# Optimization experiments

Measured on AMD Instinct MI355X. Metric: run time of the kernel, lower is better.

The kernel has to match this reference:

```python
import jax, jax.numpy as jnp
import numpy as np

D = 1024       # d_model
DR = 1024      # d_rec
FFN = 4096     # ffn_inner
K = 4          # conv_kernel
B, T = 2, 4096
CHUNK = 64
EPS = 1e-6


def setup_inputs() -> dict:
    key = jax.random.key(0)
    ks = jax.random.split(key, 8)
    s = lambda k, shape, scale: jax.random.normal(k, shape, jnp.float32) * scale
    db = np.zeros((DR,), np.float32)
    q = DR // 4
    db[:q] = -2.2
    db[q:3 * q] = 0.0
    db[3 * q:] = 4.6
    return {
        "x": s(ks[0], (B, T, D), 1.0),
        "pre_norm_w": jnp.ones((D,), jnp.float32),
        "conv_w": s(ks[1], (D, 1, K), 0.3),
        "conv_b": jnp.zeros((D,), jnp.float32),
        "w_a": s(ks[2], (DR, D), 0.02),
        "w_i": s(ks[3], (DR, D), 0.02),
        "w_v": s(ks[4], (DR, D), 0.02),
        "out_proj_w": s(ks[5], (D, DR), 0.02),
        "decay_bias": jnp.asarray(db),
        "ffn_norm_w": jnp.ones((D,), jnp.float32),
        "w_gate_up": s(ks[6], (2 * FFN, D), 0.02),
        "w_down": s(ks[7], (D, FFN), 0.02),
    }


def rmsnorm(x, w):
    return x * jax.lax.rsqrt(jnp.mean(x * x, axis=-1, keepdims=True) + EPS) * w


def lin(x, w):  # nn.Linear weight layout (out, in)
    return jnp.einsum('btd,od->bto', x, w)


def causal_conv(h, w, b):
    # depthwise causal conv: h (B,T,D), w (D,1,K)
    hc = jnp.transpose(h, (0, 2, 1))  # (B,D,T)
    out = jax.lax.conv_general_dilated(
        hc, w, window_strides=(1,), padding=[(K - 1, 0)],
        dimension_numbers=('NCH', 'OIH', 'NCH'), feature_group_count=D)
    return jnp.transpose(out, (0, 2, 1)) + b


def chunked_scan(a, v):
    b, s, d = a.shape
    pad = (-s) % CHUNK
    af = jnp.pad(a, ((0, 0), (0, pad), (0, 0)), constant_values=1.0)
    vf = jnp.pad(v, ((0, 0), (0, pad), (0, 0)))
    n = (s + pad) // CHUNK
    dc = af.reshape(b, n, CHUNK, d)
    vc = vf.reshape(b, n, CHUNK, d)
    cum_decay = jnp.exp(jnp.cumsum(jnp.log(jnp.clip(dc, 1e-10)), axis=2))
    intra = cum_decay * jnp.cumsum(vc / jnp.clip(cum_decay, 1e-10), axis=2)

    def step(state, xs):
        cd, it = xs  # (B,CHUNK,d) each
        cs = it + cd * state[:, None, :]
        return cs[:, -1], cs

    _, states = jax.lax.scan(
        step, jnp.zeros((b, d), jnp.float32),
        (jnp.transpose(cum_decay, (1, 0, 2, 3)), jnp.transpose(intra, (1, 0, 2, 3))))
    return jnp.transpose(states, (1, 0, 2, 3)).reshape(b, n * CHUNK, d)[:, :s]


def reference(x, pre_norm_w, conv_w, conv_b, w_a, w_i, w_v, out_proj_w,
              decay_bias, ffn_norm_w, w_gate_up, w_down):
    h = rmsnorm(x, pre_norm_w)
    h = causal_conv(h, conv_w, conv_b)
    a = jax.nn.sigmoid(lin(h, w_a) + decay_bias)
    i_gate = jax.nn.sigmoid(lin(h, w_i))
    v = lin(h, w_v)
    input_signal = jnp.sqrt(jnp.clip(1.0 - a * a, 1e-8)) * (i_gate * v)
    rec_out = chunked_scan(a, input_signal).astype(x.dtype)
    x = x + lin(rec_out, out_proj_w)
    hn = rmsnorm(x, ffn_norm_w)
    gu = lin(hn, w_gate_up)
    gate, up = gu[..., :FFN], gu[..., FFN:]
    x = x + lin(jax.nn.silu(gate) * up, w_down)
    return x
```

## Files before the change

kernel.cpp:

```cpp
#include <hip/hip_runtime.h>

typedef __bf16 bf16_t;
typedef bf16_t bf16x4 __attribute__((ext_vector_type(4)));
typedef bf16_t bf16x8 __attribute__((ext_vector_type(8)));
typedef float f32x4 __attribute__((ext_vector_type(4)));

#define DD 1024
#define TT 4096

__device__ __forceinline__ void gload16(const void* g, void* l) {
    __builtin_amdgcn_global_load_lds(
        (const __attribute__((address_space(1))) void*)g,
        (__attribute__((address_space(3))) void*)l, 16, 0, 0);
}

__global__ __launch_bounds__(256) void cvt_bf16_k(const float* __restrict__ s,
                                                  bf16_t* __restrict__ d, int n) {
    int i = (blockIdx.x * 256 + threadIdx.x) * 4;
    if (i < n) {
        const float4 v = *(const float4*)(s + i);
        bf16x4 o;
        o[0] = (bf16_t)v.x; o[1] = (bf16_t)v.y; o[2] = (bf16_t)v.z; o[3] = (bf16_t)v.w;
        *(bf16x4*)(d + i) = o;
    }
}

__global__ __launch_bounds__(256) void cvt_ileave_k(const float* __restrict__ s0,
                                                    const float* __restrict__ s1,
                                                    bf16_t* __restrict__ d, int total) {
    int i = (blockIdx.x * 256 + threadIdx.x) * 4;
    if (i < total) {
        const int rp = i >> 10, k = i & 1023;
        const int c = rp >> 1;
        const float* src = ((rp & 1) ? s1 : s0) + (long)c * 1024 + k;
        const float4 v = *(const float4*)src;
        bf16x4 o;
        o[0] = (bf16_t)v.x; o[1] = (bf16_t)v.y; o[2] = (bf16_t)v.z; o[3] = (bf16_t)v.w;
        *(bf16x4*)(d + i) = o;
    }
}

__global__ __launch_bounds__(256) void rmsnorm_k(const float* __restrict__ x,
                                                 const float* __restrict__ w,
                                                 bf16_t* __restrict__ ob) {
    const long row = blockIdx.x;
    const float* xr = x + row * DD;
    const int t4 = threadIdx.x * 4;
    float4 v = *(const float4*)(xr + t4);
    float s = v.x*v.x + v.y*v.y + v.z*v.z + v.w*v.w;
    #pragma unroll
    for (int off = 1; off < 64; off <<= 1) s += __shfl_xor(s, off);
    __shared__ float red[4];
    if ((threadIdx.x & 63) == 0) red[threadIdx.x >> 6] = s;
    __syncthreads();
    float tot = red[0] + red[1] + red[2] + red[3];
    float sc = rsqrtf(tot * (1.0f / DD) + 1e-6f);
    float4 wv = *(const float4*)(w + t4);
    bf16x4 o;
    o[0] = (bf16_t)(v.x*sc*wv.x); o[1] = (bf16_t)(v.y*sc*wv.y);
    o[2] = (bf16_t)(v.z*sc*wv.z); o[3] = (bf16_t)(v.w*sc*wv.w);
    *(bf16x4*)(ob + row * DD + t4) = o;
}

__global__ __launch_bounds__(256) void conv_k(const bf16_t* __restrict__ h,
                                              const float* __restrict__ cw,
                                              const float* __restrict__ cb,
                                              bf16_t* __restrict__ hc) {
    const long idx = (long)blockIdx.x * 256 + threadIdx.x;
    const int d = (int)(idx & (DD - 1));
    const long bt = idx >> 10;
    const int t = (int)(bt & (TT - 1));
    const float w0 = cw[d*4+0], w1 = cw[d*4+1], w2 = cw[d*4+2], w3 = cw[d*4+3];
    const bf16_t* hp = h + bt * DD + d;
    float acc = cb[d] + (float)hp[0] * w3;
    if (t >= 1) acc += (float)hp[-DD]     * w2;
    if (t >= 2) acc += (float)hp[-2*DD]   * w1;
    if (t >= 3) acc += (float)hp[-3*DD]   * w0;
    hc[idx] = (bf16_t)acc;
}

__global__ __launch_bounds__(256) void scan1_k(const float* __restrict__ ap,
                                               const float* __restrict__ sp,
                                               float* __restrict__ cd63,
                                               float* __restrict__ i63) {
    const int d = blockIdx.x * 256 + threadIdx.x;
    const int c = blockIdx.y;
    const int b = blockIdx.z;
    const long rowbase = (long)b * TT + (long)c * 64;
    float la = 0.0f, rs = 0.0f, cdv = 0.0f, it = 0.0f;
    for (int t = 0; t < 64; t++) {
        const long off = (rowbase + t) * DD + d;
        const float a = ap[off];
        const float s = sp[off];
        const float sig = sqrtf(fmaxf(1.0f - a * a, 1e-8f)) * s;
        la += __logf(fmaxf(a, 1e-10f));
        cdv = __expf(la);
        rs += sig / fmaxf(cdv, 1e-10f);
        it = cdv * rs;
    }
    const long o = ((long)b * 64 + c) * DD + d;
    cd63[o] = cdv;
    i63[o]  = it;
}

__global__ __launch_bounds__(256) void scan2_k(const float* __restrict__ cd63,
                                               const float* __restrict__ i63,
                                               float* __restrict__ carry_in) {
    const int g = blockIdx.x * 256 + threadIdx.x;
    const int b = g >> 10, d = g & (DD - 1);
    float st = 0.0f;
    for (int c = 0; c < 64; c++) {
        const long o = ((long)b * 64 + c) * DD + d;
        carry_in[o] = st;
        st = i63[o] + cd63[o] * st;
    }
}

__global__ __launch_bounds__(256) void scan3_k(const float* __restrict__ ap,
                                               const float* __restrict__ sp,
                                               const float* __restrict__ carry_in,
                                               bf16_t* __restrict__ rec) {
    const int d = blockIdx.x * 256 + threadIdx.x;
    const int c = blockIdx.y;
    const int b = blockIdx.z;
    const long rowbase = (long)b * TT + (long)c * 64;
    const float carry = carry_in[((long)b * 64 + c) * DD + d];
    float la = 0.0f, rs = 0.0f;
    for (int t = 0; t < 64; t++) {
        const long off = (rowbase + t) * DD + d;
        const float a = ap[off];
        const float s = sp[off];
        const float sig = sqrtf(fmaxf(1.0f - a * a, 1e-8f)) * s;
        la += __logf(fmaxf(a, 1e-10f));
        const float cdv = __expf(la);
        rs += sig / fmaxf(cdv, 1e-10f);
        rec[off] = (bf16_t)(cdv * rs + cdv * carry);
    }
}

enum { EPI_AIV = 0, EPI_ADDRES = 1, EPI_GU = 2 };

template<int EPI>
__global__ __launch_bounds__(256, 2) void gemm2b_k(const bf16_t* __restrict__ Ag,
                                                   const bf16_t* __restrict__ Bg,
                                                   int M, int N, int K,
                                                   float* outF, float* outF2,
                                                   bf16_t* outB,
                                                   const float* aux, int ldc) {
    constexpr int ASZ = 8192;
    constexpr int BUF = 16384;
    extern __shared__ bf16_t smem[];
    const int tid = threadIdx.x;
    const int l = tid & 63;
    const int w = tid >> 6;
    const int wm = w >> 1, wn = w & 1;

    const int gx = gridDim.x;
    const int gy = gridDim.y;
    const int lin = blockIdx.y * gx + blockIdx.x;
    long row0, col0;
    if ((gy & 7) == 0) {
        const int rpc = gy >> 3;
        const int q = lin >> 3;
        row0 = (long)((lin & 7) * rpc + q % rpc) * 128;
        col0 = (long)(q / rpc) * 128;
    } else {
        row0 = (long)blockIdx.y * 128;
        col0 = (long)blockIdx.x * 128;
    }

    const int srow = l >> 3;
    const int scol = ((l & 7) ^ srow) * 8;
    const long aBase = row0 + srow;
    const long bBase = col0 + srow;
    const int R0 = w * 32;

    const int NT = K >> 6;
    f32x4 acc[4][4] = {};

    const int lq2 = (l >> 4) * 16;
    const int rA = wm * 64 + (l & 15);
    const int rB = wn * 64 + (l & 15);
    const int eA0 = rA * 64 + ((lq2 ^ ((rA & 7) << 4)) >> 1);
    const int eB0 = ASZ + rB * 64 + ((lq2 ^ ((rB & 7) << 4)) >> 1);

    #define ST_A(tt, off, i)                                                        \
        gload16(Ag + (aBase + R0 + (i) * 8) * (long)K + (long)(tt) * 64 + scol,     \
                &smem[(off) + (R0 + (i) * 8) * 64])
    #define ST_B(tt, off, i)                                                        \
        gload16(Bg + (bBase + R0 + (i) * 8) * (long)K + (long)(tt) * 64 + scol,     \
                &smem[(off) + ASZ + (R0 + (i) * 8) * 64])
    #define BAR asm volatile("s_barrier" ::: "memory")

    #pragma unroll
    for (int i = 0; i < 4; i++) ST_B(0, 0, i);
    #pragma unroll
    for (int i = 0; i < 4; i++) ST_A(0, 0, i);
    #pragma unroll
    for (int i = 0; i < 4; i++) ST_B(1, BUF, i);
    asm volatile("s_waitcnt vmcnt(4)" ::: "memory");
    BAR;

    for (int t = 0; t < NT; t++) {
        const int cur = (t & 1) * BUF;
        const int oth = BUF - cur;
        bf16x8 bk[4], af[4];

        #pragma unroll
        for (int n = 0; n < 4; n++)
            bk[n] = *(const bf16x8*)&smem[cur + eB0 + n * 1024];
        #pragma unroll
        for (int m = 0; m < 4; m++)
            af[m] = *(const bf16x8*)&smem[cur + eA0 + m * 1024];
        if (t + 1 < NT) {
            #pragma unroll
            for (int i = 0; i < 4; i++) ST_A(t + 1, oth, i);
        }
        BAR;
        __builtin_amdgcn_s_setprio(1);
        #pragma unroll
        for (int m = 0; m < 4; m++)
            #pragma unroll
            for (int n = 0; n < 4; n++)
                acc[m][n] = __builtin_amdgcn_mfma_f32_16x16x32_bf16(af[m], bk[n], acc[m][n], 0, 0, 0);
        __builtin_amdgcn_s_setprio(0);
        BAR;

        #pragma unroll
        for (int n = 0; n < 4; n++)
            bk[n] = *(const bf16x8*)&smem[cur + (eB0 ^ 32) + n * 1024];
        #pragma unroll
        for (int m = 0; m < 4; m++)
            af[m] = *(const bf16x8*)&smem[cur + (eA0 ^ 32) + m * 1024];
        BAR;
        __builtin_amdgcn_s_setprio(1);
        #pragma unroll
        for (int m = 0; m < 4; m++)
            #pragma unroll
            for (int n = 0; n < 4; n++)
                acc[m][n] = __builtin_amdgcn_mfma_f32_16x16x32_bf16(af[m], bk[n], acc[m][n], 0, 0, 0);
        __builtin_amdgcn_s_setprio(0);
        if (t + 2 < NT) {
            #pragma unroll
            for (int i = 0; i < 4; i++) ST_B(t + 2, cur, i);
            asm volatile("s_waitcnt vmcnt(4)" ::: "memory");
        } else {
            asm volatile("s_waitcnt vmcnt(0)" ::: "memory");
        }
        BAR;
    }
    #undef ST_A
    #undef ST_B
    #undef BAR

    #pragma unroll
    for (int m = 0; m < 4; m++) {
        const long r0 = row0 + wm * 64 + m * 16 + (l >> 4) * 4;
        #pragma unroll
        for (int n = 0; n < 4; n++) {
            const long cc = col0 + wn * 64 + n * 16 + (l & 15);
            f32x4 v = acc[m][n];
            #pragma unroll
            for (int j = 0; j < 4; j++) {
                const long r = r0 + j;
                const float xv = v[j];
                if (EPI == EPI_AIV) {
                    if (cc < 1024) {
                        outF[r * ldc + cc] = 1.0f / (1.0f + __expf(-(xv + aux[cc])));
                    } else {
                        const float px = __shfl_xor(xv, 1);
                        if ((l & 1) == 0)
                            outF2[r * ldc + ((cc - 1024) >> 1)] = px / (1.0f + __expf(-xv));
                    }
                } else if (EPI == EPI_ADDRES) {
                    outF[r * ldc + cc] = xv + aux[r * ldc + cc];
                } else {
                    const float px = __shfl_xor(xv, 1);
                    if ((l & 1) == 0)
                        outB[r * ldc + (cc >> 1)] = (bf16_t)(xv / (1.0f + __expf(-xv)) * px);
                }
            }
        }
    }
}

extern "C" void kernel_launch(void* const* d_in, const int* in_sizes, int n_in,
                              void* d_out, int out_size, void* d_ws, size_t ws_size,
                              hipStream_t stream) {
    const float* x   = (const float*)d_in[0];
    const float* pnw = (const float*)d_in[1];
    const float* cw  = (const float*)d_in[2];
    const float* cb  = (const float*)d_in[3];
    const float* wa  = (const float*)d_in[4];
    const float* wi  = (const float*)d_in[5];
    const float* wv  = (const float*)d_in[6];
    const float* wop = (const float*)d_in[7];
    const float* db  = (const float*)d_in[8];
    const float* fnw = (const float*)d_in[9];
    const float* wgu = (const float*)d_in[10];
    const float* wdn = (const float*)d_in[11];
    float* out = (float*)d_out;

    char* ws = (char*)d_ws;
    bf16_t* wab   = (bf16_t*)(ws + 0);
    bf16_t* wivb  = (bf16_t*)(ws + 2097152);
    bf16_t* wopb  = (bf16_t*)(ws + 6291456);
    bf16_t* wgub  = (bf16_t*)(ws + 8388608);
    bf16_t* wdnb  = (bf16_t*)(ws + 25165824);
    bf16_t* hb    = (bf16_t*)(ws + 33554432);
    bf16_t* hn    = hb;
    bf16_t* hc    = (bf16_t*)(ws + 50331648);
    bf16_t* rec   = hc;
    float*  a_p   = (float*)(ws + 67108864);
    float*  s_p   = (float*)(ws + 100663296);
    bf16_t* act   = (bf16_t*)(ws + 67108864);
    float*  cd63  = (float*)(ws + 134217728);
    float*  i63   = (float*)(ws + 134742016);
    float*  carry = (float*)(ws + 135266304);

    const int LDSB = 65536;
    hipFuncSetAttribute((const void*)gemm2b_k<EPI_AIV>,    hipFuncAttributeMaxDynamicSharedMemorySize, LDSB);
    hipFuncSetAttribute((const void*)gemm2b_k<EPI_ADDRES>, hipFuncAttributeMaxDynamicSharedMemorySize, LDSB);
    hipFuncSetAttribute((const void*)gemm2b_k<EPI_GU>,     hipFuncAttributeMaxDynamicSharedMemorySize, LDSB);

    cvt_bf16_k  <<<1024, 256, 0, stream>>>(wa,  wab,  1048576);
    cvt_ileave_k<<<2048, 256, 0, stream>>>(wi,  wv, wivb, 2097152);
    cvt_bf16_k  <<<1024, 256, 0, stream>>>(wop, wopb, 1048576);
    cvt_ileave_k<<<8192, 256, 0, stream>>>(wgu, wgu + 4194304, wgub, 8388608);
    cvt_bf16_k  <<<4096, 256, 0, stream>>>(wdn, wdnb, 4194304);

    rmsnorm_k<<<8192, 256, 0, stream>>>(x, pnw, hb);
    conv_k<<<32768, 256, 0, stream>>>(hb, cw, cb, hc);

    gemm2b_k<EPI_AIV><<<dim3(24, 64), 256, LDSB, stream>>>(hc, wab, 8192, 3072, 1024,
                                                           a_p, s_p, nullptr, db, 1024);
    scan1_k<<<dim3(4, 64, 2), 256, 0, stream>>>(a_p, s_p, cd63, i63);
    scan2_k<<<8, 256, 0, stream>>>(cd63, i63, carry);
    scan3_k<<<dim3(4, 64, 2), 256, 0, stream>>>(a_p, s_p, carry, rec);

    gemm2b_k<EPI_ADDRES><<<dim3(8, 64), 256, LDSB, stream>>>(rec, wopb, 8192, 1024, 1024,
                                                             out, nullptr, nullptr, x, 1024);
    rmsnorm_k<<<8192, 256, 0, stream>>>(out, fnw, hn);
    gemm2b_k<EPI_GU><<<dim3(64, 64), 256, LDSB, stream>>>(hn, wgub, 8192, 8192, 1024,
                                                          nullptr, nullptr, act, nullptr, 4096);
    gemm2b_k<EPI_ADDRES><<<dim3(8, 64), 256, LDSB, stream>>>(act, wdnb, 8192, 1024, 4096,
                                                             out, nullptr, nullptr, out, 1024);
}
```

Measured before the change: 484.0 us.

## Switch GEMMs to 32x32x16 MFMA with new LDS layout; store input signal as bf16

```diff
diff --git a/kernel.cpp b/kernel.cpp
--- a/kernel.cpp
+++ b/kernel.cpp
@@ -4,6 +4,7 @@
 typedef bf16_t bf16x4 __attribute__((ext_vector_type(4)));
 typedef bf16_t bf16x8 __attribute__((ext_vector_type(8)));
 typedef float f32x4 __attribute__((ext_vector_type(4)));
+typedef float f32x16 __attribute__((ext_vector_type(16)));
 
 #define DD 1024
 #define TT 4096
@@ -80,7 +81,7 @@
 }
 
 __global__ __launch_bounds__(256) void scan1_k(const float* __restrict__ ap,
-                                               const float* __restrict__ sp,
+                                               const bf16_t* __restrict__ sp,
                                                float* __restrict__ cd63,
                                                float* __restrict__ i63) {
     const int d = blockIdx.x * 256 + threadIdx.x;
@@ -91,7 +92,7 @@
     for (int t = 0; t < 64; t++) {
         const long off = (rowbase + t) * DD + d;
         const float a = ap[off];
-        const float s = sp[off];
+        const float s = (float)sp[off];
         const float sig = sqrtf(fmaxf(1.0f - a * a, 1e-8f)) * s;
         la += __logf(fmaxf(a, 1e-10f));
         cdv = __expf(la);
@@ -117,7 +118,7 @@
 }
 
 __global__ __launch_bounds__(256) void scan3_k(const float* __restrict__ ap,
-                                               const float* __restrict__ sp,
+                                               const bf16_t* __restrict__ sp,
                                                const float* __restrict__ carry_in,
                                                bf16_t* __restrict__ rec) {
     const int d = blockIdx.x * 256 + threadIdx.x;
@@ -129,7 +130,7 @@
     for (int t = 0; t < 64; t++) {
         const long off = (rowbase + t) * DD + d;
         const float a = ap[off];
-        const float s = sp[off];
+        const float s = (float)sp[off];
         const float sig = sqrtf(fmaxf(1.0f - a * a, 1e-8f)) * s;
         la += __logf(fmaxf(a, 1e-10f));
         const float cdv = __expf(la);
@@ -141,14 +142,13 @@
 enum { EPI_AIV = 0, EPI_ADDRES = 1, EPI_GU = 2 };
 
 template<int EPI>
-__global__ __launch_bounds__(256, 2) void gemm2b_k(const bf16_t* __restrict__ Ag,
+__global__ __launch_bounds__(256, 2) void gemm32_k(const bf16_t* __restrict__ Ag,
                                                    const bf16_t* __restrict__ Bg,
                                                    int M, int N, int K,
-                                                   float* outF, float* outF2,
-                                                   bf16_t* outB,
+                                                   float* outF, bf16_t* outB,
                                                    const float* aux, int ldc) {
-    constexpr int ASZ = 8192;
-    constexpr int BUF = 16384;
+    constexpr int ASZE = 8192;
+    constexpr int BUFE = 16384;
     extern __shared__ bf16_t smem[];
     const int tid = threadIdx.x;
     const int l = tid & 63;
@@ -169,80 +169,86 @@
         col0 = (long)blockIdx.x * 128;
     }
 
-    const int srow = l >> 3;
-    const int scol = ((l & 7) ^ srow) * 8;
-    const long aBase = row0 + srow;
-    const long bBase = col0 + srow;
-    const int R0 = w * 32;
-
     const int NT = K >> 6;
-    f32x4 acc[4][4] = {};
-
-    const int lq2 = (l >> 4) * 16;
-    const int rA = wm * 64 + (l & 15);
-    const int rB = wn * 64 + (l & 15);
-    const int eA0 = rA * 64 + ((lq2 ^ ((rA & 7) << 4)) >> 1);
-    const int eB0 = ASZ + rB * 64 + ((lq2 ^ ((rB & 7) << 4)) >> 1);
-
-    #define ST_A(tt, off, i)                                                        \
-        gload16(Ag + (aBase + R0 + (i) * 8) * (long)K + (long)(tt) * 64 + scol,     \
-                &smem[(off) + (R0 + (i) * 8) * 64])
-    #define ST_B(tt, off, i)                                                        \
-        gload16(Bg + (bBase + R0 + (i) * 8) * (long)K + (long)(tt) * 64 + scol,     \
-                &smem[(off) + ASZ + (R0 + (i) * 8) * 64])
+    f32x16 acc[2][2] = {};
+
+    const int aRd = (l >> 5) * 1024 + (wm * 64 + (l & 31)) * 8;
+    const int bRd = ASZE + (l >> 5) * 1024 + (wn * 64 + (l & 31)) * 8;
+
+    const bf16_t* pA[4];
+    const bf16_t* pB[4];
+    #pragma unroll
+    for (int j = 0; j < 4; j++) {
+        pA[j] = Ag + (row0 + (j & 1) * 64 + l) * (long)K + (w * 2 + (j >> 1)) * 8;
+        pB[j] = Bg + (col0 + (j & 1) * 64 + l) * (long)K + (w * 2 + (j >> 1)) * 8;
+    }
+
+    #define ST_A(off) { _Pragma("unroll")                                          \
+        for (int j = 0; j < 4; j++)                                                \
+            gload16(pA[j], &smem[(off) + (w * 4 + j) * 512]);                      \
+        _Pragma("unroll")                                                          \
+        for (int j = 0; j < 4; j++) pA[j] += 64; }
+    #define ST_B(off) { _Pragma("unroll")                                          \
+        for (int j = 0; j < 4; j++)                                                \
+            gload16(pB[j], &smem[(off) + ASZE + (w * 4 + j) * 512]);               \
+        _Pragma("unroll")                                                          \
+        for (int j = 0; j < 4; j++) pB[j] += 64; }
     #define BAR asm volatile("s_barrier" ::: "memory")
 
-    #pragma unroll
-    for (int i = 0; i < 4; i++) ST_B(0, 0, i);
-    #pragma unroll
-    for (int i = 0; i < 4; i++) ST_A(0, 0, i);
-    #pragma unroll
-    for (int i = 0; i < 4; i++) ST_B(1, BUF, i);
+    ST_B(0); ST_A(0); ST_B(BUFE);
     asm volatile("s_waitcnt vmcnt(4)" ::: "memory");
     BAR;
 
     for (int t = 0; t < NT; t++) {
-        const int cur = (t & 1) * BUF;
-        const int oth = BUF - cur;
-        bf16x8 bk[4], af[4];
-
-        #pragma unroll
-        for (int n = 0; n < 4; n++)
-            bk[n] = *(const bf16x8*)&smem[cur + eB0 + n * 1024];
-        #pragma unroll
-        for (int m = 0; m < 4; m++)
-            af[m] = *(const bf16x8*)&smem[cur + eA0 + m * 1024];
-        if (t + 1 < NT) {
-            #pragma unroll
-            for (int i = 0; i < 4; i++) ST_A(t + 1, oth, i);
+        const int cur = (t & 1) * BUFE;
+        const int oth = BUFE - cur;
+        bf16x8 af[2][2], bf[2][2];
+
+        #pragma unroll
+        for (int ks = 0; ks < 2; ks++) {
+            #pragma unroll
+            for (int mb = 0; mb < 2; mb++)
+                af[ks][mb] = *(const bf16x8*)&smem[cur + aRd + ks * 2048 + mb * 256];
+            #pragma unroll
+            for (int nb = 0; nb < 2; nb++)
+                bf[ks][nb] = *(const bf16x8*)&smem[cur + bRd + ks * 2048 + nb * 256];
+        }
+        if (t + 1 < NT) { ST_A(oth); }
+        BAR;
+        __builtin_amdgcn_s_setprio(1);
+        #pragma unroll
+        for (int ks = 0; ks < 2; ks++)
+            #pragma unroll
+            for (int mb = 0; mb < 2; mb++)
+                #pragma unroll
+                for (int nb = 0; nb < 2; nb++)
+                    acc[mb][nb] = __builtin_amdgcn_mfma_f32_32x32x16_bf16(
+                        af[ks][mb], bf[ks][nb], acc[mb][nb], 0, 0, 0);
+        __builtin_amdgcn_s_setprio(0);
+        BAR;
+
+        #pragma unroll
+        for (int ks = 0; ks < 2; ks++) {
+            #pragma unroll
+            for (int mb = 0; mb < 2; mb++)
+                af[ks][mb] = *(const bf16x8*)&smem[cur + aRd + (ks + 2) * 2048 + mb * 256];
+            #pragma unroll
+            for (int nb = 0; nb < 2; nb++)
+                bf[ks][nb] = *(const bf16x8*)&smem[cur + bRd + (ks + 2) * 2048 + nb * 256];
         }
         BAR;
         __builtin_amdgcn_s_setprio(1);
         #pragma unroll
-        for (int m = 0; m < 4; m++)
-            #pragma unroll
-            for (int n = 0; n < 4; n++)
-                acc[m][n] = __builtin_amdgcn_mfma_f32_16x16x32_bf16(af[m], bk[n], acc[m][n], 0, 0, 0);
-        __builtin_amdgcn_s_setprio(0);
-        BAR;
-
-        #pragma unroll
-        for (int n = 0; n < 4; n++)
-            bk[n] = *(const bf16x8*)&smem[cur + (eB0 ^ 32) + n * 1024];
-        #pragma unroll
-        for (int m = 0; m < 4; m++)
-            af[m] = *(const bf16x8*)&smem[cur + (eA0 ^ 32) + m * 1024];
-        BAR;
-        __builtin_amdgcn_s_setprio(1);
-        #pragma unroll
-        for (int m = 0; m < 4; m++)
-            #pragma unroll
-            for (int n = 0; n < 4; n++)
-                acc[m][n] = __builtin_amdgcn_mfma_f32_16x16x32_bf16(af[m], bk[n], acc[m][n], 0, 0, 0);
+        for (int ks = 0; ks < 2; ks++)
+            #pragma unroll
+            for (int mb = 0; mb < 2; mb++)
+                #pragma unroll
+                for (int nb = 0; nb < 2; nb++)
+                    acc[mb][nb] = __builtin_amdgcn_mfma_f32_32x32x16_bf16(
+                        af[ks][mb], bf[ks][nb], acc[mb][nb], 0, 0, 0);
         __builtin_amdgcn_s_setprio(0);
         if (t + 2 < NT) {
-            #pragma unroll
-            for (int i = 0; i < 4; i++) ST_B(t + 2, cur, i);
+            ST_B(cur);
             asm volatile("s_waitcnt vmcnt(4)" ::: "memory");
         } else {
             asm volatile("s_waitcnt vmcnt(0)" ::: "memory");
@@ -254,30 +260,30 @@
     #undef BAR
 
     #pragma unroll
-    for (int m = 0; m < 4; m++) {
-        const long r0 = row0 + wm * 64 + m * 16 + (l >> 4) * 4;
-        #pragma unroll
-        for (int n = 0; n < 4; n++) {
-            const long cc = col0 + wn * 64 + n * 16 + (l & 15);
-            f32x4 v = acc[m][n];
-            #pragma unroll
-            for (int j = 0; j < 4; j++) {
-                const long r = r0 + j;
-                const float xv = v[j];
+    for (int mb = 0; mb < 2; mb++) {
+        #pragma unroll
+        for (int nb = 0; nb < 2; nb++) {
+            const long cc = col0 + wn * 64 + nb * 32 + (l & 31);
+            f32x16 v = acc[mb][nb];
+            #pragma unroll
+            for (int r = 0; r < 16; r++) {
+                const long rr = row0 + wm * 64 + mb * 32 + (r & 3) + 8 * (r >> 2) + 4 * (l >> 5);
+                const float xv = v[r];
                 if (EPI == EPI_AIV) {
                     if (cc < 1024) {
-                        outF[r * ldc + cc] = 1.0f / (1.0f + __expf(-(xv + aux[cc])));
+                        outF[rr * ldc + cc] = 1.0f / (1.0f + __expf(-(xv + aux[cc])));
                     } else {
                         const float px = __shfl_xor(xv, 1);
                         if ((l & 1) == 0)
-                            outF2[r * ldc + ((cc - 1024) >> 1)] = px / (1.0f + __expf(-xv));
+                            outB[rr * ldc + ((cc - 1024) >> 1)] =
+                                (bf16_t)(px / (1.0f + __expf(-xv)));
                     }
                 } else if (EPI == EPI_ADDRES) {
-                    outF[r * ldc + cc] = xv + aux[r * ldc + cc];
+                    outF[rr * ldc + cc] = xv + aux[rr * ldc + cc];
                 } else {
                     const float px = __shfl_xor(xv, 1);
                     if ((l & 1) == 0)
-                        outB[r * ldc + (cc >> 1)] = (bf16_t)(xv / (1.0f + __expf(-xv)) * px);
+                        outB[rr * ldc + (cc >> 1)] = (bf16_t)(xv / (1.0f + __expf(-xv)) * px);
                 }
             }
         }
@@ -312,16 +318,16 @@
     bf16_t* hc    = (bf16_t*)(ws + 50331648);
     bf16_t* rec   = hc;
     float*  a_p   = (float*)(ws + 67108864);
-    float*  s_p   = (float*)(ws + 100663296);
+    bf16_t* s_b   = (bf16_t*)(ws + 100663296);
     bf16_t* act   = (bf16_t*)(ws + 67108864);
     float*  cd63  = (float*)(ws + 134217728);
     float*  i63   = (float*)(ws + 134742016);
     float*  carry = (float*)(ws + 135266304);
 
     const int LDSB = 65536;
-    hipFuncSetAttribute((const void*)gemm2b_k<EPI_AIV>,    hipFuncAttributeMaxDynamicSharedMemorySize, LDSB);
-    hipFuncSetAttribute((const void*)gemm2b_k<EPI_ADDRES>, hipFuncAttributeMaxDynamicSharedMemorySize, LDSB);
-    hipFuncSetAttribute((const void*)gemm2b_k<EPI_GU>,     hipFuncAttributeMaxDynamicSharedMemorySize, LDSB);
+    hipFuncSetAttribute((const void*)gemm32_k<EPI_AIV>,    hipFuncAttributeMaxDynamicSharedMemorySize, LDSB);
+    hipFuncSetAttribute((const void*)gemm32_k<EPI_ADDRES>, hipFuncAttributeMaxDynamicSharedMemorySize, LDSB);
+    hipFuncSetAttribute((const void*)gemm32_k<EPI_GU>,     hipFuncAttributeMaxDynamicSharedMemorySize, LDSB);
 
     cvt_bf16_k  <<<1024, 256, 0, stream>>>(wa,  wab,  1048576);
     cvt_ileave_k<<<2048, 256, 0, stream>>>(wi,  wv, wivb, 2097152);
@@ -332,17 +338,17 @@
     rmsnorm_k<<<8192, 256, 0, stream>>>(x, pnw, hb);
     conv_k<<<32768, 256, 0, stream>>>(hb, cw, cb, hc);
 
-    gemm2b_k<EPI_AIV><<<dim3(24, 64), 256, LDSB, stream>>>(hc, wab, 8192, 3072, 1024,
-                                                           a_p, s_p, nullptr, db, 1024);
-    scan1_k<<<dim3(4, 64, 2), 256, 0, stream>>>(a_p, s_p, cd63, i63);
+    gemm32_k<EPI_AIV><<<dim3(24, 64), 256, LDSB, stream>>>(hc, wab, 8192, 3072, 1024,
+                                                           a_p, s_b, db, 1024);
+    scan1_k<<<dim3(4, 64, 2), 256, 0, stream>>>(a_p, s_b, cd63, i63);
     scan2_k<<<8, 256, 0, stream>>>(cd63, i63, carry);
-    scan3_k<<<dim3(4, 64, 2), 256, 0, stream>>>(a_p, s_p, carry, rec);
-
-    gemm2b_k<EPI_ADDRES><<<dim3(8, 64), 256, LDSB, stream>>>(rec, wopb, 8192, 1024, 1024,
-                                                             out, nullptr, nullptr, x, 1024);
+    scan3_k<<<dim3(4, 64, 2), 256, 0, stream>>>(a_p, s_b, carry, rec);
+
+    gemm32_k<EPI_ADDRES><<<dim3(8, 64), 256, LDSB, stream>>>(rec, wopb, 8192, 1024, 1024,
+                                                             out, nullptr, x, 1024);
     rmsnorm_k<<<8192, 256, 0, stream>>>(out, fnw, hn);
-    gemm2b_k<EPI_GU><<<dim3(64, 64), 256, LDSB, stream>>>(hn, wgub, 8192, 8192, 1024,
-                                                          nullptr, nullptr, act, nullptr, 4096);
-    gemm2b_k<EPI_ADDRES><<<dim3(8, 64), 256, LDSB, stream>>>(act, wdnb, 8192, 1024, 4096,
-                                                             out, nullptr, nullptr, out, 1024);
-}
+    gemm32_k<EPI_GU><<<dim3(64, 64), 256, LDSB, stream>>>(hn, wgub, 8192, 8192, 1024,
+                                                          nullptr, act, nullptr, 4096);
+    gemm32_k<EPI_ADDRES><<<dim3(8, 64), 256, LDSB, stream>>>(act, wdnb, 8192, 1024, 4096,
+                                                             out, nullptr, out, 1024);
+}
```

Measured after the change: 680.3 us. 1.41x slower.
